# Kernel tuning notes

Measured on AMD Instinct MI355X. Metric: run time of the kernel, lower is better.

## Reference

```python
import jax, jax.numpy as jnp
import numpy as np

B, S, D, H = 4, 1024, 1024, 16
HD = D // H          # head space dim = 64
FF = 4 * D           # ffn hidden = 4096
EPS = 1e-6

# ---- Lorentz manifold helpers (curvature k=1: -t^2 + |s|^2 = -1) ----

def to_manifold(space):
    t = jnp.sqrt(jnp.sum(space * space, -1, keepdims=True) + 1.0)
    return jnp.concatenate([t, space], -1)

def l_inner(x, y):
    return -x[..., 0] * y[..., 0] + jnp.sum(x[..., 1:] * y[..., 1:], -1)

def project(z):
    # renormalize onto hyperboloid: z / sqrt(|<z,z>_L|)   (Lorentz midpoint / LResNet)
    d = jnp.sqrt(jnp.clip(-l_inner(z, z), EPS))
    return z / d[..., None]

def hyp_layernorm(x, g, b):
    s = x[..., 1:]
    mu = jnp.mean(s, -1, keepdims=True)
    var = jnp.var(s, -1, keepdims=True)
    s = (s - mu) * jax.lax.rsqrt(var + 1e-5) * g + b
    return to_manifold(s)

def apply_rope(xs, cos, sin):
    # xs [B,S,H,HD]; cos/sin [S,HD//2]; freqs broadcast as [1,S,1,HD//2]
    x2 = xs.reshape(*xs.shape[:-1], HD // 2, 2)
    c = cos[None, :, None, :]
    s = sin[None, :, None, :]
    xr = x2[..., 0] * c - x2[..., 1] * s
    xi = x2[..., 0] * s + x2[..., 1] * c
    return jnp.stack([xr, xi], -1).reshape(xs.shape)


def setup_inputs() -> dict:
    key = jax.random.key(0)
    ks = jax.random.split(key, 8)
    def w(k, shape, fan_in):
        return jax.random.normal(k, shape, jnp.float32) / np.sqrt(fan_in).astype(np.float32)
    x = to_manifold(0.5 * jax.random.normal(ks[0], (B, S, D), jnp.float32))
    pos = jnp.arange(S, dtype=jnp.float32)[:, None]
    inv = 1.0 / (10000.0 ** (jnp.arange(0, HD, 2, dtype=jnp.float32) / HD))
    ang = pos * inv[None, :]
    return {
        'x': x,
        'rope_cos': jnp.cos(ang), 'rope_sin': jnp.sin(ang),
        'norm1_g': jnp.ones((D,), jnp.float32), 'norm1_b': jnp.zeros((D,), jnp.float32),
        'Wq': w(ks[1], (H, D + 1, HD), D + 1), 'bq': jnp.zeros((H, HD), jnp.float32),
        'Wk': w(ks[2], (H, D + 1, HD), D + 1), 'bk': jnp.zeros((H, HD), jnp.float32),
        'Wv': w(ks[3], (H, D + 1, HD), D + 1), 'bv': jnp.zeros((H, HD), jnp.float32),
        'attn_scale': jnp.asarray(np.sqrt(HD), jnp.float32),
        'attn_bias': jnp.zeros((), jnp.float32),
        'Wo': w(ks[4], (H * (HD + 1), D), H * (HD + 1)), 'bo': jnp.zeros((D,), jnp.float32),
        'w_res1': jnp.asarray(1.0, jnp.float32),
        'norm2_g': jnp.ones((D,), jnp.float32), 'norm2_b': jnp.zeros((D,), jnp.float32),
        'W1': w(ks[5], (D + 1, FF), D + 1), 'b1': jnp.zeros((FF,), jnp.float32),
        'W2': w(ks[6], (FF + 1, D), FF + 1), 'b2': jnp.zeros((D,), jnp.float32),
        'w_res2': jnp.asarray(1.0, jnp.float32),
    }


def reference(x, rope_cos, rope_sin, norm1_g, norm1_b, Wq, bq, Wk, bk, Wv, bv,
              attn_scale, attn_bias, Wo, bo, w_res1, norm2_g, norm2_b,
              W1, b1, W2, b2, w_res2):
    # ---- pre-norm ----
    xn = hyp_layernorm(x, norm1_g, norm1_b)
    # ---- per-head Lorentz linear (space part), inline RoPE on q/k ----
    qs = jnp.einsum('bsd,hde->bshe', xn, Wq) + bq          # [B,S,H,HD]
    ksp = jnp.einsum('bsd,hde->bshe', xn, Wk) + bk
    vsp = jnp.einsum('bsd,hde->bshe', xn, Wv) + bv
    qs = apply_rope(qs, rope_cos, rope_sin)
    ksp = apply_rope(ksp, rope_cos, rope_sin)
    # hyperbolic normalization of q/k: unit space norm, time recomputed
    qs = qs * jax.lax.rsqrt(jnp.sum(qs * qs, -1, keepdims=True) + EPS)
    ksp = ksp * jax.lax.rsqrt(jnp.sum(ksp * ksp, -1, keepdims=True) + EPS)
    q = to_manifold(qs)                                    # [B,S,H,HD+1]
    k = to_manifold(ksp)
    v = to_manifold(vsp)
    # ---- curvature-aware scores: 2 + 2 <q,k>_L (neg sq Lorentz distance) ----
    sgn = jnp.concatenate([-jnp.ones((1,), q.dtype), jnp.ones((HD,), q.dtype)])
    cin = jnp.einsum('bshe,bthe->bhst', q * sgn, k)        # Minkowski inner [B,H,S,S]
    att = (2.0 + 2.0 * cin) / attn_scale + attn_bias
    P = jax.nn.softmax(att, axis=-1)
    # ---- Lorentz midpoint aggregation of values ----
    m = jnp.einsum('bhst,bthe->bshe', P, v)
    m = project(m)                                         # back onto hyperboloid
    # ---- heads concat + output Lorentz linear ----
    cat = m.reshape(B, S, H * (HD + 1))
    attn_out = to_manifold(cat @ Wo + bo)
    # ---- LResNet residual 1 ----
    x = project(x + w_res1 * attn_out)
    # ---- Lorentz FFN ----
    h = hyp_layernorm(x, norm2_g, norm2_b)
    h = to_manifold(jax.nn.gelu(h @ W1 + b1))
    mlp = to_manifold(h @ W2 + b2)
    # ---- LResNet residual 2 ----
    x = project(x + w_res2 * mlp)
    return x
```

## Files before the change

kernel.cpp:

```cpp
#include <hip/hip_runtime.h>
#include <hip/hip_bf16.h>

typedef __hip_bfloat16 bf16;
typedef __attribute__((ext_vector_type(8))) short short8;
typedef __attribute__((ext_vector_type(4))) float f32x4;

#define B_  4
#define S_  1024
#define H_  16
#define R_  4096
#define LD_ 1088

#define MBL 1048576L
#define OFF_WQKVT (0L)
#define OFF_WOT   (6684672L)
#define OFF_X2    (0L)
#define OFF_W1T   (9L*MBL)
#define OFF_W2T   (18L*MBL)
#define OFF_BIAS  (26L*MBL)
#define OFF_XNB   (27L*MBL + MBL/2)
#define OFF_MCAT  OFF_XNB
#define OFF_HBUF  OFF_XNB
#define OFF_QPS   (36L*MBL)
#define OFF_ARAW  OFF_QPS
#define OFF_KPS   (44L*MBL)
#define OFF_VT    (52L*MBL)
#define OFF_QT    (62L*MBL)
#define OFF_KT    (62L*MBL + 262144L)
#define OFF_HHBIG (44L*MBL)
#define OFF_MLPB  (76L*MBL)
#define OFF_HHC   (36L*MBL)
#define OFF_MLPF  (44L*MBL)
#define BQKV 0
#define BOF  16384
#define B1F  32768
#define B2F  65536
#define W2R0 81920
#define RCF  98304
#define RSNF 262144
#define SCLF 409600
#define TACC 425984
#define FLAG 458752

__device__ __forceinline__ bf16  f2bf(float v) { return __float2bfloat16(v); }
__device__ __forceinline__ float bf2f(bf16 v)  { return __bfloat162float(v); }
__device__ __forceinline__ unsigned short bf2s(float v) {
  return __builtin_bit_cast(unsigned short, __float2bfloat16(v));
}
__device__ __forceinline__ float ldu(const void* p, long i, int isbf) {
  return isbf ? bf2f(((const bf16*)p)[i]) : ((const float*)p)[i];
}
__device__ __forceinline__ void stu(void* p, long i, float v, int isbf) {
  if (isbf) ((bf16*)p)[i] = f2bf(v);
  else      ((float*)p)[i] = v;
}
__device__ __forceinline__ float gelu_f(float v) {
  const float u = 0.7978845608028654f * (v + 0.044715f * v * v * v);
  const float e = __expf(fminf(2.f * u, 80.f));
  return 0.5f * v * (1.f + (e - 1.f) / (e + 1.f));
}
__device__ __forceinline__ float bfu_lo(unsigned u) {
  return __builtin_bit_cast(float, u << 16);
}
__device__ __forceinline__ float bfu_hi(unsigned u) {
  return __builtin_bit_cast(float, u & 0xFFFF0000u);
}

__device__ __forceinline__ void gload16(const bf16* g, short* l) {
  __builtin_amdgcn_global_load_lds(
      (const __attribute__((address_space(1))) unsigned int*)g,
      (__attribute__((address_space(3))) unsigned int*)l, 16, 0, 0);
}

#define MFMA_(acc_, a_, b_) acc_ = __builtin_amdgcn_mfma_f32_16x16x32_bf16(a_, b_, acc_, 0, 0, 0)
#define LGKM_GUARD() do { \
    asm volatile("s_waitcnt lgkmcnt(0)" ::: "memory"); \
    __builtin_amdgcn_sched_barrier(0); \
  } while (0)

__global__ void detect_kernel(const unsigned* __restrict__ g, int* __restrict__ flag) {
  if (threadIdx.x == 0) flag[0] = (g[0] == 0x3F803F80u) ? 1 : 0;
}

__global__ __launch_bounds__(256) void zero16_kernel(uint4* __restrict__ p, int n16) {
  int i = blockIdx.x * 256 + threadIdx.x;
  if (i < n16) p[i] = uint4{0, 0, 0, 0};
}

__device__ __forceinline__ float bred_f(float v, float* sh) {
#pragma unroll
  for (int o = 32; o; o >>= 1) v += __shfl_xor(v, o);
  __syncthreads();
  if ((threadIdx.x & 63) == 0) sh[threadIdx.x >> 6] = v;
  __syncthreads();
  return sh[0] + sh[1] + sh[2] + sh[3];
}
__device__ __forceinline__ double bred_d(double v, double* sh) {
#pragma unroll
  for (int o = 32; o; o >>= 1) v += __shfl_xor(v, o);
  __syncthreads();
  if ((threadIdx.x & 63) == 0) sh[threadIdx.x >> 6] = v;
  __syncthreads();
  return sh[0] + sh[1] + sh[2] + sh[3];
}

__global__ __launch_bounds__(256) void mega_prep(
    const void* x, const void* rc, const void* rsn, const void* n1g, const void* n1b,
    const void* Wq, const void* bq, const void* Wk, const void* bk,
    const void* Wv, const void* bv, const void* scl, const void* ab,
    const void* Wo, const void* bo, const void* wr1,
    const void* W1, const void* b1, const void* W2, const void* b2, const void* wr2,
    char* bias_base, bf16* __restrict__ wqkvT, bf16* __restrict__ woT,
    bf16* __restrict__ w1T, bf16* __restrict__ w2T, bf16* __restrict__ xnb,
    const int* __restrict__ flag) {
  const int isbf = flag[0];
  __shared__ float tl[64][65];
  const int tid = threadIdx.x;
  int bid = blockIdx.x;
  if (bid < 297) {
    int i = bid * 256 + tid;
    float* bqkvf = (float*)(bias_base + BQKV);
    if (i < 1024)        { bqkvf[i] = ldu(bq, i, isbf); return; }
    if (i < 2048)        { bqkvf[i] = ldu(bk, i - 1024, isbf); return; }
    if (i < 3072)        { bqkvf[i] = ldu(bv, i - 2048, isbf); return; }
    if (i < 4096)        { ((float*)(bias_base + BOF))[i - 3072] = ldu(bo, i - 3072, isbf); return; }
    if (i < 8192)        { ((float*)(bias_base + B1F))[i - 4096] = ldu(b1, i - 4096, isbf); return; }
    if (i < 9216)        { ((float*)(bias_base + B2F))[i - 8192] = ldu(b2, i - 8192, isbf); return; }
    if (i < 10240)       { ((float*)(bias_base + W2R0))[i - 9216] = ldu(W2, i - 9216, isbf); return; }
    if (i < 10240+32768) { ((float*)(bias_base + RCF))[i - 10240] = ldu(rc, i - 10240, isbf); return; }
    if (i < 10240+65536) { ((float*)(bias_base + RSNF))[i - 43008] = ldu(rsn, i - 43008, isbf); return; }
    if (i == 75776)      { ((float*)(bias_base + SCLF))[0] = ldu(scl, 0, isbf); return; }
    if (i == 75777)      { ((float*)(bias_base + SCLF))[1] = ldu(ab, 0, isbf); return; }
    if (i == 75778)      { ((float*)(bias_base + SCLF))[2] = ldu(wr1, 0, isbf); return; }
    if (i == 75779)      { ((float*)(bias_base + SCLF))[3] = ldu(wr2, 0, isbf); return; }
    return;
  }
  bid -= 297;
  const int tx = tid & 63, tg = tid >> 6;
  if (bid < 816) {
    int k0 = (bid % 17) * 64, z = bid / 17;
    int mode = z >> 4, h = z & 15;
    const void* src = (mode == 0) ? Wq : (mode == 1) ? Wk : Wv;
    const long soff = (long)h * 1025 * 64;
    int base_n = mode * 1024 + h * 64;
    for (int i = tg; i < 64; i += 4) {
      int k = k0 + i;
      tl[i][tx] = (k < 1025) ? ldu(src, soff + (long)k * 64 + tx, isbf) : 0.f;
    }
    __syncthreads();
    for (int i = tg; i < 64; i += 4) {
      int k = k0 + tx;
      if (k < LD_) wqkvT[(long)(base_n + i) * LD_ + k] = f2bf(tl[tx][i]);
    }
    return;
  }
  bid -= 816;
  if (bid < 272) {
    int k0 = (bid % 17) * 64, n0 = (bid / 17) * 64;
    for (int i = tg; i < 64; i += 4) {
      int kp = k0 + i;
      float v = 0.f;
      if (kp < 1056) {
        int h = kp / 66, e = kp - h * 66;
        if (e < 65) v = ldu(Wo, (long)(h * 65 + e) * 1024 + n0 + tx, isbf);
      }
      tl[i][tx] = v;
    }
    __syncthreads();
    for (int i = tg; i < 64; i += 4) {
      int kp = k0 + tx;
      if (kp < LD_) woT[(long)(n0 + i) * LD_ + kp] = f2bf(tl[tx][i]);
    }
    return;
  }
  bid -= 272;
  if (bid < 1088) {
    int k0 = (bid % 17) * 64, n0 = (bid / 17) * 64;
    for (int i = tg; i < 64; i += 4) {
      int k = k0 + i;
      tl[i][tx] = (k < 1025) ? ldu(W1, (long)k * 4096 + n0 + tx, isbf) : 0.f;
    }
    __syncthreads();
    for (int i = tg; i < 64; i += 4) {
      int k = k0 + tx;
      if (k < LD_) w1T[(long)(n0 + i) * LD_ + k] = f2bf(tl[tx][i]);
    }
    return;
  }
  bid -= 1088;
  if (bid < 1024) {
    int k0 = (bid % 64) * 64, n0 = (bid / 64) * 64;
    for (int i = tg; i < 64; i += 4) {
      int k = k0 + i;
      tl[i][tx] = ldu(W2, 1024 + (long)k * 1024 + n0 + tx, isbf);
    }
    __syncthreads();
    for (int i = tg; i < 64; i += 4) {
      int k = k0 + tx;
      w2T[(long)(n0 + i) * 4096 + k] = f2bf(tl[tx][i]);
    }
    return;
  }
  bid -= 1024;
  {
    float* red = &tl[0][0];
    const long base = (long)bid * 1025;
    const long obase = (long)bid * LD_;
    float v[4];
#pragma unroll
    for (int i = 0; i < 4; i++) v[i] = ldu(x, base + 1 + tid * 4 + i, isbf);
    float s = 0.f, s2 = 0.f;
#pragma unroll
    for (int i = 0; i < 4; i++) { s += v[i]; s2 += v[i] * v[i]; }
    s  = bred_f(s,  red);
    s2 = bred_f(s2, red);
    const float mu  = s * (1.f / 1024.f);
    const float var = s2 * (1.f / 1024.f) - mu * mu;
    const float rs  = rsqrtf(var + 1e-5f);
    float n[4], ns = 0.f;
#pragma unroll
    for (int i = 0; i < 4; i++) {
      const int e = tid * 4 + i;
      n[i] = (v[i] - mu) * rs * ldu(n1g, e, isbf) + ldu(n1b, e, isbf);
      ns += n[i] * n[i];
    }
    ns = bred_f(ns, red);
    if (tid == 0) xnb[obase] = f2bf(sqrtf(ns + 1.f));
#pragma unroll
    for (int i = 0; i < 4; i++) xnb[obase + 1 + tid * 4 + i] = f2bf(n[i]);
    if (tid < 63) xnb[obase + 1025 + tid] = f2bf(0.f);
  }
}

#define BUFS 16384
__device__ __forceinline__ void g256_main(const bf16* __restrict__ A, int lda,
                                          const bf16* __restrict__ Bw, int ldb, int K,
                                          short* __restrict__ AsB, short* __restrict__ BsB,
                                          f32x4 (*acc)[4]) {
  const int tid = threadIdx.x, lane = tid & 63, wv = tid >> 6;
  const int quad = lane >> 4, q15 = lane & 15;
  const int wm = wv >> 2, wn = wv & 3;
  const int m0 = blockIdx.y * 256, n0 = blockIdx.x * 256;
  const int NT = K >> 6;
  const int srow = tid >> 3;
  const int sunit = (tid & 7) ^ (srow & 7);
  const bf16* pa[4]; const bf16* pb[4];
#pragma unroll
  for (int j = 0; j < 4; j++) {
    pa[j] = A  + (long)(m0 + j * 64 + srow) * lda + sunit * 8;
    pb[j] = Bw + (long)(n0 + j * 64 + srow) * ldb + sunit * 8;
  }
#pragma unroll
  for (int j = 0; j < 4; j++) gload16(pa[j], AsB + (j * 512 + tid) * 8);
#pragma unroll
  for (int j = 0; j < 4; j++) gload16(pb[j], BsB + (j * 512 + tid) * 8);
#pragma unroll
  for (int j = 0; j < 4; j++) { pb[j] += 64; gload16(pb[j], BsB + BUFS + (j * 512 + tid) * 8); }
#pragma unroll
  for (int j = 0; j < 4; j++) { pa[j] += 64; pb[j] += 64; }
  asm volatile("s_waitcnt vmcnt(4)" ::: "memory");
  __builtin_amdgcn_s_barrier();
  const int aoff = wm * 128 * 64 + q15 * 64;
  const int boff = wn * 64 * 64 + q15 * 64;
  const int rd0 = ((quad) ^ (q15 & 7)) * 8;
  const int rd1 = ((4 + quad) ^ (q15 & 7)) * 8;
#pragma unroll 1
  for (int t = 0; t < NT; t++) {
    const int c = t & 1;
    const short* Ab = AsB + c * BUFS;
    const short* Bb = BsB + c * BUFS;
    short* Ast = AsB + (c ^ 1) * BUFS;
    short* Bst = BsB + c * BUFS;
    short8 af[4][2], b01[2][2], b23[2][2];
#pragma unroll
    for (int f = 0; f < 4; f++) {
      af[f][0] = *(const short8*)(Ab + aoff + f * 16 * 64 + rd0);
      af[f][1] = *(const short8*)(Ab + aoff + f * 16 * 64 + rd1);
    }
#pragma unroll
    for (int g = 0; g < 2; g++) {
      b01[g][0] = *(const short8*)(Bb + boff + g * 16 * 64 + rd0);
      b01[g][1] = *(const short8*)(Bb + boff + g * 16 * 64 + rd1);
    }
    if (t + 1 < NT) {
#pragma unroll
      for (int j = 0; j < 4; j++) gload16(pa[j], Ast + (j * 512 + tid) * 8);
#pragma unroll
      for (int j = 0; j < 4; j++) pa[j] += 64;
    }
    __builtin_amdgcn_s_barrier();
    __builtin_amdgcn_s_setprio(1);
#pragma unroll
    for (int kk = 0; kk < 2; kk++)
#pragma unroll
      for (int f = 0; f < 4; f++)
#pragma unroll
        for (int g = 0; g < 2; g++)
          MFMA_(acc[f][g], af[f][kk], b01[g][kk]);
    __builtin_amdgcn_s_setprio(0);
    __builtin_amdgcn_s_barrier();
#pragma unroll
    for (int g = 0; g < 2; g++) {
      b23[g][0] = *(const short8*)(Bb + boff + (32 + g * 16) * 64 + rd0);
      b23[g][1] = *(const short8*)(Bb + boff + (32 + g * 16) * 64 + rd1);
    }
    __builtin_amdgcn_s_barrier();
    __builtin_amdgcn_s_setprio(1);
#pragma unroll
    for (int kk = 0; kk < 2; kk++)
#pragma unroll
      for (int f = 0; f < 4; f++)
#pragma unroll
        for (int g = 0; g < 2; g++)
          MFMA_(acc[f][2 + g], af[f][kk], b23[g][kk]);
    __builtin_amdgcn_s_setprio(0);
    LGKM_GUARD();
    __builtin_amdgcn_s_barrier();
#pragma unroll
    for (int f = 0; f < 4; f++) {
      af[f][0] = *(const short8*)(Ab + aoff + (64 + f * 16) * 64 + rd0);
      af[f][1] = *(const short8*)(Ab + aoff + (64 + f * 16) * 64 + rd1);
    }
    if (t + 2 < NT) {
      gload16(pb[0], Bst + (0 * 512 + tid) * 8);
      gload16(pb[1], Bst + (1 * 512 + tid) * 8);
    }
    __builtin_amdgcn_s_barrier();
    __builtin_amdgcn_s_setprio(1);
#pragma unroll
    for (int kk = 0; kk < 2; kk++)
#pragma unroll
      for (int f = 0; f < 4; f++)
#pragma unroll
        for (int g = 0; g < 2; g++)
          MFMA_(acc[4 + f][g], af[f][kk], b01[g][kk]);
    __builtin_amdgcn_s_setprio(0);
    __builtin_amdgcn_s_barrier();
    if (t + 2 < NT) {
      gload16(pb[2], Bst + (2 * 512 + tid) * 8);
      gload16(pb[3], Bst + (3 * 512 + tid) * 8);
#pragma unroll
      for (int j = 0; j < 4; j++) pb[j] += 64;
    }
    __builtin_amdgcn_s_setprio(1);
#pragma unroll
    for (int kk = 0; kk < 2; kk++)
#pragma unroll
      for (int f = 0; f < 4; f++)
#pragma unroll
        for (int g = 0; g < 2; g++)
          MFMA_(acc[4 + f][2 + g], af[f][kk], b23[g][kk]);
    __builtin_amdgcn_s_setprio(0);
    if (t + 2 < NT) {
      asm volatile("s_waitcnt vmcnt(4) lgkmcnt(0)" ::: "memory");
    } else {
      asm volatile("s_waitcnt vmcnt(0) lgkmcnt(0)" ::: "memory");
    }
    __builtin_amdgcn_sched_barrier(0);
    __builtin_amdgcn_s_barrier();
  }
}

template <int EPI>
__global__ __launch_bounds__(512) void gemm256(const bf16* __restrict__ A, int lda,
                                               const bf16* __restrict__ Bw, int ldb, int K,
                                               const float* __restrict__ bias,
                                               void* __restrict__ Cv, int ldc, int accf) {
  __shared__ __align__(16) short As[2][BUFS];
  __shared__ __align__(16) short Bs[2][BUFS];
  f32x4 acc[8][4] = {};
  g256_main(A, lda, Bw, ldb, K, &As[0][0], &Bs[0][0], acc);
  const int tid = threadIdx.x, lane = tid & 63, wv = tid >> 6;
  const int quad = lane >> 4, q15 = lane & 15;
  const int wave_m = wv >> 2, wave_n = wv & 3;
  const int m0 = blockIdx.y * 256, n0 = blockIdx.x * 256;
#pragma unroll
  for (int j = 0; j < 8; j++) {
#pragma unroll
    for (int r = 0; r < 4; r++) {
      const int m = m0 + wave_m * 128 + j * 16 + quad * 4 + r;
#pragma unroll
      for (int ni = 0; ni < 4; ni++) {
        const int n = n0 + wave_n * 64 + ni * 16 + q15;
        float v = acc[j][ni][r] + (bias ? bias[n] : 0.f);
        const long idx = (long)m * ldc + n;
        if (EPI == 0) {
          float* Cf = (float*)Cv;
          if (accf) v += Cf[idx];
          Cf[idx] = v;
        } else if (EPI == 1) {
          ((bf16*)Cv)[idx] = f2bf(v);
        } else {
          ((bf16*)Cv)[idx] = f2bf(gelu_f(v));
        }
      }
    }
  }
}

__global__ __launch_bounds__(512) void gemm_qkv256(const bf16* __restrict__ A,
                                                   const bf16* __restrict__ Wt,
                                                   const char* __restrict__ bias_base,
                                                   bf16* __restrict__ qPs, float* __restrict__ qtc,
                                                   bf16* __restrict__ kPs, float* __restrict__ ktc,
                                                   bf16* __restrict__ vT) {
  __shared__ __align__(16) short As[2][BUFS];
  __shared__ __align__(16) short Bs[2][BUFS];
  f32x4 acc[8][4] = {};
  g256_main(A, LD_, Wt, LD_, LD_, &As[0][0], &Bs[0][0], acc);
  const int tid = threadIdx.x, lane = tid & 63, wv = tid >> 6;
  const int quad = lane >> 4, q15 = lane & 15;
  const int wave_m = wv >> 2, wave_n = wv & 3;
  const int m0 = blockIdx.y * 256, n0 = blockIdx.x * 256;
  const float* bqkvf = (const float*)(bias_base + BQKV);
  const float* rcf   = (const float*)(bias_base + RCF);
  const float* rsnf  = (const float*)(bias_base + RSNF);
  const int hg = (n0 >> 6) + wave_n;
  const int mode = hg >> 4, h = hg & 15;
  const int nb = hg * 64;
#pragma unroll
  for (int j = 0; j < 8; j++) {
#pragma unroll
    for (int r = 0; r < 4; r++) {
      const int m = m0 + wave_m * 128 + j * 16 + quad * 4 + r;
      const int bb = m >> 10, s = m & 1023;
      const int bh = bb * H_ + h;
      float v[4];
#pragma unroll
      for (int ns = 0; ns < 4; ns++) v[ns] = acc[j][ns][r] + bqkvf[nb + ns * 16 + q15];
      if (mode < 2) {
#pragma unroll
        for (int ns = 0; ns < 4; ns++) {
          const int eg = ns * 16 + q15;
          const int jj = eg >> 1;
          const float c = rcf[s * 32 + jj], sn = rsnf[s * 32 + jj];
          const float p = __shfl_xor(v[ns], 1);
          v[ns] = ((eg & 1) == 0) ? (v[ns] * c - p * sn) : (p * sn + v[ns] * c);
        }
      }
      float ss = v[0] * v[0] + v[1] * v[1] + v[2] * v[2] + v[3] * v[3];
#pragma unroll
      for (int o = 8; o; o >>= 1) ss += __shfl_xor(ss, o);
      if (mode == 0) {
        const float sc = rsqrtf(ss + 1e-6f);
        const long rb2 = (long)(bh * 1024 + s) * 64;
#pragma unroll
        for (int ns = 0; ns < 4; ns++) qPs[rb2 + ns * 16 + q15] = f2bf(v[ns] * sc);
        if (q15 == 0) qtc[bh * 1024 + s] = sqrtf(ss / (ss + 1e-6f) + 1.f);
      } else if (mode == 1) {
        const float sc = rsqrtf(ss + 1e-6f);
        const long rb2 = (long)(bh * 1024 + s) * 64;
#pragma unroll
        for (int ns = 0; ns < 4; ns++) kPs[rb2 + ns * 16 + q15] = f2bf(v[ns] * sc);
        if (q15 == 0) ktc[bh * 1024 + s] = sqrtf(ss / (ss + 1e-6f) + 1.f);
      } else {
        const long vb = (long)bh * 81920;
#pragma unroll
        for (int ns = 0; ns < 4; ns++) vT[vb + (long)(1 + ns * 16 + q15) * 1024 + s] = f2bf(v[ns]);
        if (q15 == 0) vT[vb + s] = f2bf(sqrtf(ss + 1.f));
      }
    }
  }
}

template <int EPI, bool SS>
__global__ __launch_bounds__(256) void mfma_gemm(const bf16* __restrict__ A, int lda,
                                                 const bf16* __restrict__ Bw, int ldb, int K,
                                                 const float* __restrict__ bias,
                                                 void* __restrict__ Cv, int ldc, int accf,
                                                 float* __restrict__ tacc) {
  __shared__ __align__(16) short As[2][128 * 32];
  __shared__ __align__(16) short Bs[2][64 * 32];
  const int tid = threadIdx.x, lane = tid & 63, wv = tid >> 6;
  const int quad = lane >> 4, q15 = lane & 15;
  const int wave_m = wv & 1, wave_n = wv >> 1;
  const int n0 = blockIdx.x * 64, m0 = blockIdx.y * 128;
  const int sa0 = wv * 128 + lane, sa1 = sa0 + 64;
  const int ra0 = sa0 >> 2, ca0 = (sa0 & 3) ^ (ra0 & 3);
  const int ra1 = sa1 >> 2, ca1 = (sa1 & 3) ^ (ra1 & 3);
  const int rb = tid >> 2, cb = (tid & 3) ^ (rb & 3);
  const int kswz = (quad ^ (q15 & 3)) * 8;
  const bf16* pa0 = A + (long)(m0 + ra0) * lda + ca0 * 8;
  const bf16* pa1 = A + (long)(m0 + ra1) * lda + ca1 * 8;
  const bf16* pb  = Bw + (long)(n0 + rb) * ldb + cb * 8;
  f32x4 acc[4][2] = {};
  for (int k0 = 0; k0 < K; k0 += 64) {
#pragma unroll
    for (int p = 0; p < 2; p++) {
      gload16(pa0 + p * 32, As[p] + sa0 * 8);
      gload16(pa1 + p * 32, As[p] + sa1 * 8);
      gload16(pb + p * 32, Bs[p] + tid * 8);
    }
    pa0 += 64; pa1 += 64; pb += 64;
    __syncthreads();
#pragma unroll
    for (int p = 0; p < 2; p++) {
      short8 af[4], bfr[2];
#pragma unroll
      for (int i = 0; i < 4; i++)
        af[i] = *(const short8*)(As[p] + (wave_m * 64 + i * 16 + q15) * 32 + kswz);
#pragma unroll
      for (int i = 0; i < 2; i++)
        bfr[i] = *(const short8*)(Bs[p] + (wave_n * 32 + i * 16 + q15) * 32 + kswz);
#pragma unroll
      for (int mi = 0; mi < 4; mi++)
#pragma unroll
        for (int ni = 0; ni < 2; ni++)
          acc[mi][ni] = __builtin_amdgcn_mfma_f32_16x16x32_bf16(af[mi], bfr[ni], acc[mi][ni], 0, 0, 0);
    }
    __syncthreads();
  }
#pragma unroll
  for (int mi = 0; mi < 4; mi++) {
#pragma unroll
    for (int r = 0; r < 4; r++) {
      const int m = m0 + wave_m * 64 + mi * 16 + quad * 4 + r;
      float s2 = 0.f;
#pragma unroll
      for (int ni = 0; ni < 2; ni++) {
        const int n = n0 + wave_n * 32 + ni * 16 + q15;
        float v = acc[mi][ni][r] + (bias ? bias[n] : 0.f);
        const long idx = (long)m * ldc + n;
        if (EPI == 0) {
          float* Cf = (float*)Cv;
          if (accf) v += Cf[idx];
          Cf[idx] = v;
        } else if (EPI == 1) {
          ((bf16*)Cv)[idx] = f2bf(v);
        } else {
          v = gelu_f(v);
          ((bf16*)Cv)[idx] = f2bf(v);
        }
        if (SS) s2 += v * v;
      }
      if (SS) {
        s2 += __shfl_xor(s2, 1);
        s2 += __shfl_xor(s2, 2);
        s2 += __shfl_xor(s2, 4);
        s2 += __shfl_xor(s2, 8);
        if (q15 == 0) atomicAdd(tacc + m, s2);
      }
    }
  }
}

__global__ __launch_bounds__(256) void attn_kernel(const bf16* __restrict__ qPs,
                                                   const float* __restrict__ qtc,
                                                   const bf16* __restrict__ kPs,
                                                   const float* __restrict__ ktc,
                                                   const bf16* __restrict__ vT,
                                                   const float* __restrict__ scalf,
                                                   bf16* __restrict__ mcat) {
  __shared__ __align__(16) short kbuf[64 * 72];
  __shared__ __align__(16) short vbuf[80 * 72];
  __shared__ __align__(16) short pbuf[64 * 72];
  __shared__ float tkl[64];
  const int tid = threadIdx.x, lane = tid & 63, wv = tid >> 6;
  const int quad = lane >> 4, q15 = lane & 15;
  const int id = blockIdx.x;
  const int cxd = id & 7, jj_ = id >> 3;
  const int bh = cxd * 8 + (jj_ & 7), qt_ = jj_ >> 3;
  const float inv_scale = 1.f / scalf[0];
  const long qrow = (long)(bh * 1024 + qt_ * 64 + wv * 16 + q15) * 64;
  const short8 aq0 = *(const short8*)(qPs + qrow + quad * 8);
  const short8 aq1 = *(const short8*)(qPs + qrow + 32 + quad * 8);
  float tqr[4];
#pragma unroll
  for (int r = 0; r < 4; r++) tqr[r] = qtc[bh * 1024 + qt_ * 64 + wv * 16 + quad * 4 + r];
  f32x4 out[5];
#pragma unroll
  for (int mt = 0; mt < 5; mt++) out[mt] = f32x4{0, 0, 0, 0};
  float lip[4] = {0.f, 0.f, 0.f, 0.f};
  const int srcl = (q15 >> 2) << 4;
  for (int kt = 0; kt < 16; kt++) {
    __syncthreads();
#pragma unroll
    for (int c = 0; c < 2; c++) {
      const int id2 = c * 256 + tid, row = id2 >> 3, off = id2 & 7;
      *(uint4*)(kbuf + row * 72 + off * 8) =
          *(const uint4*)(kPs + (long)(bh * 1024 + kt * 64 + row) * 64 + off * 8);
    }
#pragma unroll
    for (int c = 0; c < 3; c++) {
      const int id2 = c * 256 + tid;
      if (id2 < 640) {
        const int row = id2 >> 3, off = id2 & 7;
        *(uint4*)(vbuf + row * 72 + off * 8) =
            *(const uint4*)(vT + (long)bh * 81920 + (long)row * 1024 + kt * 64 + off * 8);
      }
    }
    if (tid < 64) tkl[tid] = ktc[bh * 1024 + kt * 64 + tid];
    __syncthreads();
    f32x4 sacc[4] = {f32x4{0,0,0,0}, f32x4{0,0,0,0}, f32x4{0,0,0,0}, f32x4{0,0,0,0}};
#pragma unroll
    for (int ns = 0; ns < 4; ns++) {
      short8 b0 = *(const short8*)(kbuf + (ns * 16 + q15) * 72 + quad * 8);
      short8 b1 = *(const short8*)(kbuf + (ns * 16 + q15) * 72 + 32 + quad * 8);
      sacc[ns] = __builtin_amdgcn_mfma_f32_16x16x32_bf16(aq0, b0, sacc[ns], 0, 0, 0);
      sacc[ns] = __builtin_amdgcn_mfma_f32_16x16x32_bf16(aq1, b1, sacc[ns], 0, 0, 0);
    }
#pragma unroll
    for (int ns = 0; ns < 4; ns++) {
      const float tk = tkl[ns * 16 + q15];
#pragma unroll
      for (int r = 0; r < 4; r++) {
        const float pv = __expf((2.f + 2.f * (sacc[ns][r] - tqr[r] * tk)) * inv_scale);
        lip[r] += pv;
        pbuf[(wv * 16 + quad * 4 + r) * 72 + ns * 16 + q15] = (short)bf2s(pv);
      }
    }
#pragma unroll
    for (int mt = 0; mt < 5; mt++)
#pragma unroll
      for (int kc = 0; kc < 2; kc++) {
        short8 av = *(const short8*)(vbuf + (mt * 16 + q15) * 72 + kc * 32 + quad * 8);
        short8 bp = *(const short8*)(pbuf + (wv * 16 + q15) * 72 + kc * 32 + quad * 8);
        out[mt] = __builtin_amdgcn_mfma_f32_16x16x32_bf16(av, bp, out[mt], 0, 0, 0);
      }
  }
  {
#pragma unroll
    for (int o = 8; o; o >>= 1)
#pragma unroll
      for (int r = 0; r < 4; r++) lip[r] += __shfl_xor(lip[r], o);
    float linv[4];
#pragma unroll
    for (int r = 0; r < 4; r++) linv[r] = 1.f / lip[r];
    const float t0 = __shfl(linv[0], srcl), t1 = __shfl(linv[1], srcl);
    const float t2 = __shfl(linv[2], srcl), t3 = __shfl(linv[3], srcl);
    const int rr = q15 & 3;
    const float lv = (rr == 0) ? t0 : (rr == 1) ? t1 : (rr == 2) ? t2 : t3;
#pragma unroll
    for (int mt = 0; mt < 5; mt++)
#pragma unroll
      for (int j = 0; j < 4; j++) out[mt][j] *= lv;
  }
  float part = 0.f;
#pragma unroll
  for (int mt = 0; mt < 5; mt++)
#pragma unroll
    for (int j = 0; j < 4; j++) {
      const int e = mt * 16 + quad * 4 + j;
      const float vv = out[mt][j] * out[mt][j];
      part += (e == 0) ? vv : -vv;
    }
  part += __shfl_xor(part, 16);
  part += __shfl_xor(part, 32);
  const float dinv = rsqrtf(fmaxf(part, 1e-6f));
  __syncthreads();
  short* obuf = vbuf;
  const int qrow_l = wv * 16 + q15;
#pragma unroll
  for (int mt = 0; mt < 5; mt++)
#pragma unroll
    for (int j = 0; j < 4; j++) {
      const int e = mt * 16 + quad * 4 + j;
      if (e <= 64) obuf[qrow_l * 72 + e] = (short)bf2s(out[mt][j] * dinv);
    }
  if (quad == 1) obuf[qrow_l * 72 + 65] = 0;
  __syncthreads();
  const int b = bh >> 4, h = bh & 15;
  const long outbase = ((long)b * 1024 + qt_ * 64) * LD_ + h * 66;
  for (int i = tid; i < 64 * 33; i += 256) {
    const int row = i / 33, p = i - row * 33;
    *(unsigned*)(mcat + outbase + (long)row * LD_ + p * 2) =
        *(const unsigned*)(obuf + row * 72 + p * 2);
  }
  if (h == 15) {
    const long zb = ((long)b * 1024 + qt_ * 64) * LD_ + 1056;
    for (int i = tid; i < 64 * 16; i += 256) {
      const int row = i >> 4, p = i & 15;
      *(unsigned*)(mcat + zb + (long)row * LD_ + p * 2) = 0u;
    }
  }
}

__global__ __launch_bounds__(256) void final_fix_kernel(const float* __restrict__ t_acc,
                                                        const float* __restrict__ w2r0,
                                                        const float* __restrict__ b2f,
                                                        float* __restrict__ mlp) {
  const int m = blockIdx.x;
  const float t = sqrtf(1.f + t_acc[m]);
  float* row = mlp + (long)m * 1024;
  for (int n = threadIdx.x; n < 1024; n += 256) row[n] += t * w2r0[n] + b2f[n];
}

__global__ __launch_bounds__(256) void final_fix_big(const bf16* __restrict__ hh,
                                                     const float* __restrict__ w2r0,
                                                     const float* __restrict__ b2f,
                                                     float* __restrict__ mlp) {
  __shared__ float red[4];
  const int m = blockIdx.x;
  const uint4* r4 = (const uint4*)(hh + (long)m * 4096);
  float ss = 0.f;
  for (int i = threadIdx.x; i < 512; i += 256) {
    const uint4 u = r4[i];
    const unsigned a[4] = {u.x, u.y, u.z, u.w};
#pragma unroll
    for (int j = 0; j < 4; j++) {
      const float lo = bfu_lo(a[j]), hi = bfu_hi(a[j]);
      ss += lo * lo + hi * hi;
    }
  }
  ss = bred_f(ss, red);
  const float t = sqrtf(1.f + ss);
  float* row = mlp + (long)m * 1024;
  for (int n = threadIdx.x; n < 1024; n += 256) row[n] += t * w2r0[n] + b2f[n];
}

__global__ __launch_bounds__(256) void proj_ln_kernel(
    const void* __restrict__ x, const bf16* __restrict__ c,
    const float* __restrict__ scalf, int widx,
    const void* __restrict__ g, const void* __restrict__ b,
    bf16* __restrict__ x2, bf16* __restrict__ hbuf, const int* __restrict__ flag) {
  const int isbf = flag[0];
  __shared__ double redd[4];
  __shared__ float redf[4];
  const long bx = (long)blockIdx.x * 1025;
  const long bc = (long)blockIdx.x * 1024;
  const long ob = (long)blockIdx.x * LD_;
  const int tid = threadIdx.x;
  const double w = (double)scalf[widx];
  const float x0 = ldu(x, bx, isbf);
  float xs[4], cv[4];
#pragma unroll
  for (int i = 0; i < 4; i++) {
    xs[i] = ldu(x, bx + 1 + tid * 4 + i, isbf);
    cv[i] = bf2f(c[bc + tid * 4 + i]);
  }
  double cc = 0.0, xx = 0.0, xc = 0.0, sx = 0.0, sc_ = 0.0;
#pragma unroll
  for (int i = 0; i < 4; i++) {
    cc += (double)cv[i] * cv[i];
    xx += (double)xs[i] * xs[i];
    xc += (double)xs[i] * cv[i];
    sx += (double)xs[i];
    sc_ += (double)cv[i];
  }
  cc = bred_d(cc, redd);
  xx = bred_d(xx, redd);
  xc = bred_d(xc, redd);
  sx = bred_d(sx, redd);
  sc_ = bred_d(sc_, redd);
  const double t   = sqrt(1.0 + cc);
  const double lxx = (double)x0 * x0 - xx;
  const double xm  = -(double)x0 * t + xc;
  double d2 = lxx + w * w - 2.0 * w * xm;
  if (d2 < 1e-6) d2 = 1e-6;
  const double dinv = 1.0 / sqrt(d2);
  if (tid == 0) x2[bx] = f2bf((float)(((double)x0 + w * t) * dinv));
  float z[4];
#pragma unroll
  for (int i = 0; i < 4; i++) {
    z[i] = (float)(((double)xs[i] + w * cv[i]) * dinv);
    x2[bx + 1 + tid * 4 + i] = f2bf(z[i]);
  }
  const float sumz  = (float)((sx + w * sc_) * dinv);
  const float sumsq = (float)((xx + 2.0 * w * xc + w * w * cc) * dinv * dinv);
  const float mu  = sumz * (1.f / 1024.f);
  const float var = sumsq * (1.f / 1024.f) - mu * mu;
  const float rs  = rsqrtf(var + 1e-5f);
  float n[4], ns = 0.f;
#pragma unroll
  for (int i = 0; i < 4; i++) {
    const int e = tid * 4 + i;
    n[i] = (z[i] - mu) * rs * ldu(g, e, isbf) + ldu(b, e, isbf);
    ns += n[i] * n[i];
  }
  ns = bred_f(ns, redf);
  if (tid == 0) hbuf[ob] = f2bf(sqrtf(ns + 1.f));
#pragma unroll
  for (int i = 0; i < 4; i++) hbuf[ob + 1 + tid * 4 + i] = f2bf(n[i]);
  if (tid < 63) hbuf[ob + 1025 + tid] = f2bf(0.f);
}

__global__ __launch_bounds__(256) void res_project_kernel(
    const void* __restrict__ x, int xtag, const void* __restrict__ c, int ctag,
    const float* __restrict__ scalf, int widx, void* __restrict__ out, int otag,
    const int* __restrict__ flag) {
  const int isbf = flag[0];
  const int xb = (xtag == 2) ? isbf : xtag;
  const int cb2 = (ctag == 2) ? isbf : ctag;
  const int ob = (otag == 2) ? isbf : otag;
  __shared__ double red[4];
  const long bx = (long)blockIdx.x * 1025;
  const long bc = (long)blockIdx.x * 1024;
  const int tid = threadIdx.x;
  const double w = (double)scalf[widx];
  const float x0 = ldu(x, bx, xb);
  float xs[4], cv[4];
#pragma unroll
  for (int i = 0; i < 4; i++) {
    xs[i] = ldu(x, bx + 1 + tid * 4 + i, xb);
    cv[i] = ldu(c, bc + tid * 4 + i, cb2);
  }
  double cc = 0.0, xx = 0.0, xc = 0.0;
#pragma unroll
  for (int i = 0; i < 4; i++) {
    cc += (double)cv[i] * cv[i];
    xx += (double)xs[i] * xs[i];
    xc += (double)xs[i] * cv[i];
  }
  cc = bred_d(cc, red);
  xx = bred_d(xx, red);
  xc = bred_d(xc, red);
  const double t   = sqrt(1.0 + cc);
  const double lxx = (double)x0 * x0 - xx;
  const double xm  = -(double)x0 * t + xc;
  double d2 = lxx + w * w - 2.0 * w * xm;
  if (d2 < 1e-6) d2 = 1e-6;
  const double dinv = 1.0 / sqrt(d2);
  if (tid == 0) stu(out, bx, (float)(((double)x0 + w * t) * dinv), ob);
#pragma unroll
  for (int i = 0; i < 4; i++)
    stu(out, bx + 1 + tid * 4 + i, (float)(((double)xs[i] + w * cv[i]) * dinv), ob);
}

extern "C" void kernel_launch(void* const* d_in, const int* in_sizes, int n_in,
                              void* d_out, int out_size, void* d_ws, size_t ws_size,
                              hipStream_t stream) {
  char* w = (char*)d_ws;
  char* bias_base = w + OFF_BIAS;
  int* flag = (int*)(bias_base + FLAG);
  float* tacc = (float*)(bias_base + TACC);
  const float* scalf = (const float*)(bias_base + SCLF);
  const bool big = ws_size >= (size_t)92 * MBL;
  char* mlp_off = big ? (w + OFF_MLPB) : (w + OFF_MLPF);

  detect_kernel<<<1, 64, 0, stream>>>((const unsigned*)d_in[3], flag);
  zero16_kernel<<<4, 256, 0, stream>>>((uint4*)tacc, 1024);

  mega_prep<<<7593, 256, 0, stream>>>(
      d_in[0], d_in[1], d_in[2], d_in[3], d_in[4], d_in[5], d_in[6], d_in[7], d_in[8],
      d_in[9], d_in[10], d_in[11], d_in[12], d_in[13], d_in[14], d_in[15], d_in[18],
      d_in[19], d_in[20], d_in[21], d_in[22], bias_base, (bf16*)(w + OFF_WQKVT),
      (bf16*)(w + OFF_WOT), (bf16*)(w + OFF_W1T), (bf16*)(w + OFF_W2T),
      (bf16*)(w + OFF_XNB), flag);

  gemm_qkv256<<<dim3(12, 16), 512, 0, stream>>>(
      (const bf16*)(w + OFF_XNB), (const bf16*)(w + OFF_WQKVT), bias_base,
      (bf16*)(w + OFF_QPS), (float*)(w + OFF_QT), (bf16*)(w + OFF_KPS),
      (float*)(w + OFF_KT), (bf16*)(w + OFF_VT));
  attn_kernel<<<1024, 256, 0, stream>>>(
      (const bf16*)(w + OFF_QPS), (const float*)(w + OFF_QT), (const bf16*)(w + OFF_KPS),
      (const float*)(w + OFF_KT), (const bf16*)(w + OFF_VT), scalf, (bf16*)(w + OFF_MCAT));
  mfma_gemm<1, false><<<dim3(16, 32), 256, 0, stream>>>(
      (const bf16*)(w + OFF_MCAT), LD_, (const bf16*)(w + OFF_WOT), LD_, LD_,
      (const float*)(bias_base + BOF), w + OFF_ARAW, 1024, 0, nullptr);
  proj_ln_kernel<<<R_, 256, 0, stream>>>(d_in[0], (const bf16*)(w + OFF_ARAW), scalf, 2,
                                         d_in[16], d_in[17], (bf16*)(w + OFF_X2),
                                         (bf16*)(w + OFF_HBUF), flag);
  if (big) {
    gemm256<2><<<dim3(16, 16), 512, 0, stream>>>(
        (const bf16*)(w + OFF_HBUF), LD_, (const bf16*)(w + OFF_W1T), LD_, LD_,
        (const float*)(bias_base + B1F), w + OFF_HHBIG, 4096, 0);
    mfma_gemm<0, false><<<dim3(16, 32), 256, 0, stream>>>(
        (const bf16*)(w + OFF_HHBIG), 4096, (const bf16*)(w + OFF_W2T), 4096, 4096,
        nullptr, mlp_off, 1024, 0, nullptr);
    final_fix_big<<<R_, 256, 0, stream>>>((const bf16*)(w + OFF_HHBIG),
                                          (const float*)(bias_base + W2R0),
                                          (const float*)(bias_base + B2F),
                                          (float*)mlp_off);
  } else {
    for (int c = 0; c < 4; c++) {
      mfma_gemm<2, true><<<dim3(16, 32), 256, 0, stream>>>(
          (const bf16*)(w + OFF_HBUF), LD_, (const bf16*)(w + OFF_W1T) + (long)c * 1024 * LD_,
          LD_, LD_, (const float*)(bias_base + B1F) + c * 1024, w + OFF_HHC, 1024, 0, tacc);
      mfma_gemm<0, false><<<dim3(16, 32), 256, 0, stream>>>(
          (const bf16*)(w + OFF_HHC), 1024, (const bf16*)(w + OFF_W2T) + c * 1024, 4096, 1024,
          nullptr, mlp_off, 1024, c > 0 ? 1 : 0, nullptr);
    }
    final_fix_kernel<<<R_, 256, 0, stream>>>(tacc, (const float*)(bias_base + W2R0),
                                             (const float*)(bias_base + B2F),
                                             (float*)mlp_off);
  }
  res_project_kernel<<<R_, 256, 0, stream>>>(w + OFF_X2, 1, mlp_off, 0, scalf, 3,
                                             d_out, 2, flag);
}
```

Measured before the change: 465.7 us.

## Use split-K 256-tile GEMM with atomic accumulation for the FFN down projection

Replaces the 128-tile FFN down-projection GEMM (M=4096, N=1024, K=4096) with a 256x256-tile kernel split four ways along K, 256 blocks in total. Block indices are remapped to group neighbouring tiles, and the partial sums are combined with fp32 atomicAdd into an output buffer that is zeroed beforehand. The aim is to run the larger, more efficient tile while still filling the GPU with enough blocks. The cost is an extra 16 MB zeroing pass, atomic traffic on the output, and a non-deterministic summation order. It also removes two sched_barrier calls in the shared GEMM main loop, which may change instruction scheduling for every GEMM that uses it.

```diff
diff --git a/kernel.cpp b/kernel.cpp
--- a/kernel.cpp
+++ b/kernel.cpp
@@ -73,10 +73,7 @@
 }
 
 #define MFMA_(acc_, a_, b_) acc_ = __builtin_amdgcn_mfma_f32_16x16x32_bf16(a_, b_, acc_, 0, 0, 0)
-#define LGKM_GUARD() do { \
-    asm volatile("s_waitcnt lgkmcnt(0)" ::: "memory"); \
-    __builtin_amdgcn_sched_barrier(0); \
-  } while (0)
+#define LGKM_GUARD() asm volatile("s_waitcnt lgkmcnt(0)" ::: "memory")
 
 __global__ void detect_kernel(const unsigned* __restrict__ g, int* __restrict__ flag) {
   if (threadIdx.x == 0) flag[0] = (g[0] == 0x3F803F80u) ? 1 : 0;
@@ -235,12 +232,12 @@
 #define BUFS 16384
 __device__ __forceinline__ void g256_main(const bf16* __restrict__ A, int lda,
                                           const bf16* __restrict__ Bw, int ldb, int K,
+                                          int m0, int n0,
                                           short* __restrict__ AsB, short* __restrict__ BsB,
                                           f32x4 (*acc)[4]) {
   const int tid = threadIdx.x, lane = tid & 63, wv = tid >> 6;
   const int quad = lane >> 4, q15 = lane & 15;
   const int wm = wv >> 2, wn = wv & 3;
-  const int m0 = blockIdx.y * 256, n0 = blockIdx.x * 256;
   const int NT = K >> 6;
   const int srow = tid >> 3;
   const int sunit = (tid & 7) ^ (srow & 7);
@@ -356,7 +353,6 @@
     } else {
       asm volatile("s_waitcnt vmcnt(0) lgkmcnt(0)" ::: "memory");
     }
-    __builtin_amdgcn_sched_barrier(0);
     __builtin_amdgcn_s_barrier();
   }
 }
@@ -369,11 +365,11 @@
   __shared__ __align__(16) short As[2][BUFS];
   __shared__ __align__(16) short Bs[2][BUFS];
   f32x4 acc[8][4] = {};
-  g256_main(A, lda, Bw, ldb, K, &As[0][0], &Bs[0][0], acc);
+  const int m0 = blockIdx.y * 256, n0 = blockIdx.x * 256;
+  g256_main(A, lda, Bw, ldb, K, m0, n0, &As[0][0], &Bs[0][0], acc);
   const int tid = threadIdx.x, lane = tid & 63, wv = tid >> 6;
   const int quad = lane >> 4, q15 = lane & 15;
   const int wave_m = wv >> 2, wave_n = wv & 3;
-  const int m0 = blockIdx.y * 256, n0 = blockIdx.x * 256;
 #pragma unroll
   for (int j = 0; j < 8; j++) {
 #pragma unroll
@@ -398,6 +394,36 @@
   }
 }
 
+__global__ __launch_bounds__(512) void gemm256_splitk(const bf16* __restrict__ A, int lda,
+                                                      const bf16* __restrict__ Bw, int ldb,
+                                                      int Kslice,
+                                                      float* __restrict__ Cf, int ldc) {
+  __shared__ __align__(16) short As[2][BUFS];
+  __shared__ __align__(16) short Bs[2][BUFS];
+  f32x4 acc[8][4] = {};
+  const int lin = blockIdx.x;
+  const int rmp = (lin & 7) * 32 + (lin >> 3);
+  const int x = rmp & 3, y = (rmp >> 2) & 15, z = rmp >> 6;
+  const int m0 = y * 256, n0 = x * 256;
+  const long koff = (long)z * Kslice;
+  g256_main(A + koff, lda, Bw + koff, ldb, Kslice, m0, n0, &As[0][0], &Bs[0][0], acc);
+  const int tid = threadIdx.x, lane = tid & 63, wv = tid >> 6;
+  const int quad = lane >> 4, q15 = lane & 15;
+  const int wave_m = wv >> 2, wave_n = wv & 3;
+#pragma unroll
+  for (int j = 0; j < 8; j++) {
+#pragma unroll
+    for (int r = 0; r < 4; r++) {
+      const int m = m0 + wave_m * 128 + j * 16 + quad * 4 + r;
+#pragma unroll
+      for (int ni = 0; ni < 4; ni++) {
+        const int n = n0 + wave_n * 64 + ni * 16 + q15;
+        atomicAdd(Cf + (long)m * ldc + n, acc[j][ni][r]);
+      }
+    }
+  }
+}
+
 __global__ __launch_bounds__(512) void gemm_qkv256(const bf16* __restrict__ A,
                                                    const bf16* __restrict__ Wt,
                                                    const char* __restrict__ bias_base,
@@ -407,11 +433,11 @@
   __shared__ __align__(16) short As[2][BUFS];
   __shared__ __align__(16) short Bs[2][BUFS];
   f32x4 acc[8][4] = {};
-  g256_main(A, LD_, Wt, LD_, LD_, &As[0][0], &Bs[0][0], acc);
+  const int m0 = blockIdx.y * 256, n0 = blockIdx.x * 256;
+  g256_main(A, LD_, Wt, LD_, LD_, m0, n0, &As[0][0], &Bs[0][0], acc);
   const int tid = threadIdx.x, lane = tid & 63, wv = tid >> 6;
   const int quad = lane >> 4, q15 = lane & 15;
   const int wave_m = wv >> 2, wave_n = wv & 3;
-  const int m0 = blockIdx.y * 256, n0 = blockIdx.x * 256;
   const float* bqkvf = (const float*)(bias_base + BQKV);
   const float* rcf   = (const float*)(bias_base + RCF);
   const float* rsnf  = (const float*)(bias_base + RSNF);
@@ -829,6 +855,9 @@
 
   detect_kernel<<<1, 64, 0, stream>>>((const unsigned*)d_in[3], flag);
   zero16_kernel<<<4, 256, 0, stream>>>((uint4*)tacc, 1024);
+  if (big) {
+    zero16_kernel<<<4096, 256, 0, stream>>>((uint4*)mlp_off, 1048576);
+  }
 
   mega_prep<<<7593, 256, 0, stream>>>(
       d_in[0], d_in[1], d_in[2], d_in[3], d_in[4], d_in[5], d_in[6], d_in[7], d_in[8],
@@ -854,9 +883,9 @@
     gemm256<2><<<dim3(16, 16), 512, 0, stream>>>(
         (const bf16*)(w + OFF_HBUF), LD_, (const bf16*)(w + OFF_W1T), LD_, LD_,
         (const float*)(bias_base + B1F), w + OFF_HHBIG, 4096, 0);
-    mfma_gemm<0, false><<<dim3(16, 32), 256, 0, stream>>>(
-        (const bf16*)(w + OFF_HHBIG), 4096, (const bf16*)(w + OFF_W2T), 4096, 4096,
-        nullptr, mlp_off, 1024, 0, nullptr);
+    gemm256_splitk<<<256, 512, 0, stream>>>(
+        (const bf16*)(w + OFF_HHBIG), 4096, (const bf16*)(w + OFF_W2T), 4096, 1024,
+        (float*)mlp_off, 1024);
     final_fix_big<<<R_, 256, 0, stream>>>((const bf16*)(w + OFF_HHBIG),
                                           (const float*)(bias_base + W2R0),
                                           (const float*)(bias_base + B2F),
```

New measurement: 487.6 us. 4.7% more time.
